# Optimization experiments

Hardware: AMD Instinct MI355X
Metric: run time of the kernel (lower is better)

Reference implementation:

```python
import jax, jax.numpy as jnp
import numpy as np

N, F_IN, HEADS, F_OUT = 4096, 128, 4, 32
DENSITY = 0.05


def setup_inputs() -> dict:
    key = jax.random.key(0)
    k_x, k_adj, k_w, k_as, k_ad, k_b = jax.random.split(key, 6)
    x = jax.random.normal(k_x, (N, F_IN), dtype=jnp.float32)
    # binary adjacency with self-loops so every row of Tau_sum is nonzero
    adj = (jax.random.uniform(k_adj, (N, N)) < DENSITY).astype(jnp.float32)
    adj = jnp.maximum(adj, jnp.eye(N, dtype=jnp.float32))
    weight = jax.random.normal(k_w, (HEADS * F_OUT, F_IN), dtype=jnp.float32) * 0.1
    att_src = jax.random.normal(k_as, (1, HEADS, F_OUT), dtype=jnp.float32) * 0.1
    att_dst = jax.random.normal(k_ad, (1, HEADS, F_OUT), dtype=jnp.float32) * 0.1
    bias = jax.random.normal(k_b, (HEADS * F_OUT,), dtype=jnp.float32) * 0.1
    return {"x": x, "adj_matrix": adj, "weight": weight,
            "att_src": att_src, "att_dst": att_dst, "bias": bias}


def reference(x, adj_matrix, weight, att_src, att_dst, bias):
    n = x.shape[0]
    heads = att_src.shape[1]
    f_out = weight.shape[0] // heads
    # H' = x W^T, reshaped to [N, heads, F_out]
    h_prime = (x @ weight.T).reshape(n, heads, f_out)
    alpha_src = jnp.sum(h_prime * att_src, axis=-1)  # [N, heads]
    alpha_dst = jnp.sum(h_prime * att_dst, axis=-1)  # [N, heads]
    # C[m, n, h] = alpha_src[n, h] + alpha_dst[m, h]
    C = alpha_src[None, :, :] + alpha_dst[:, None, :]
    adj_t = adj_matrix.T[..., None]                  # [N, N, 1]
    # exp(leaky_relu(C, 0.2)) masked by adjacency
    tau = adj_t * jnp.exp(jnp.maximum(0.2 * C, C))   # [N, N, heads]
    tau_sum = jnp.sum(tau, axis=1, keepdims=True)    # [N, 1, heads]
    att_weights = tau / tau_sum
    # Z[m, h, f] = sum_n (adjT * att)[m, n, h] * H'[n, h, f]
    z = jnp.einsum('mnh,nhf->mhf', adj_t * att_weights, h_prime)
    return z.reshape(n, heads * f_out) + bias
```

## Files before the change

kernel.cpp:

```cpp
#include <hip/hip_runtime.h>
#include <hip/hip_bf16.h>

#define N_NODES 4096
#define F_IN    128
#define HEADS   4
#define FTOT    128
#define NSPLIT  16
#define NRANGE  (N_NODES / NSPLIT)
#define NSTEP   (NRANGE / 64)
#define HPB     512
#define BITB    1024
#define L2E     1.4426950408889634f

typedef __attribute__((ext_vector_type(8)))  short  short8v;
typedef __attribute__((ext_vector_type(16))) float  float16v;

static __device__ __forceinline__ unsigned f2bfu(float f) {
    union { __hip_bfloat16 h; unsigned short u; } cv;
    cv.h = __float2bfloat16(f);
    return (unsigned)cv.u;
}
static __device__ __forceinline__ unsigned cvt_pk_bf16(float lo, float hi) {
    unsigned r;
    asm("v_cvt_pk_bf16_f32 %0, %1, %2" : "=v"(r) : "v"(lo), "v"(hi));
    return r;
}

__global__ __launch_bounds__(256)
void k_pre(const float* __restrict__ x, const float* __restrict__ W,
           const float* __restrict__ att_src, const float* __restrict__ att_dst,
           const float* __restrict__ adj,
           unsigned short* __restrict__ hpt, float* __restrict__ ast,
           float* __restrict__ adt, unsigned* __restrict__ abits)
{
    const int t = threadIdx.x;
    if (blockIdx.x < HPB) {
        __shared__ alignas(16) float    xs[8 * F_IN];
        __shared__ alignas(16) unsigned hs[F_IN * 4];
        __shared__ float ssa[4][8], ssd[4][8];
        const int sub = t >> 7;
        const int tt  = t & 127;
        const int i0  = blockIdx.x * 8;
        reinterpret_cast<float4*>(xs)[t] =
            reinterpret_cast<const float4*>(x + (size_t)i0 * F_IN)[t];
        __syncthreads();

        const float4* W4  = reinterpret_cast<const float4*>(W + tt * F_IN);
        const float4* xs4 = reinterpret_cast<const float4*>(xs + sub * 4 * F_IN);
        float a0 = 0.f, a1 = 0.f, a2 = 0.f, a3 = 0.f;
#pragma unroll
        for (int k = 0; k < F_IN / 4; ++k) {
            const float4 w  = W4[k];
            const float4 v0 = xs4[k], v1 = xs4[32 + k], v2 = xs4[64 + k], v3 = xs4[96 + k];
            a0 = fmaf(w.x, v0.x, a0); a0 = fmaf(w.y, v0.y, a0); a0 = fmaf(w.z, v0.z, a0); a0 = fmaf(w.w, v0.w, a0);
            a1 = fmaf(w.x, v1.x, a1); a1 = fmaf(w.y, v1.y, a1); a1 = fmaf(w.z, v1.z, a1); a1 = fmaf(w.w, v1.w, a1);
            a2 = fmaf(w.x, v2.x, a2); a2 = fmaf(w.y, v2.y, a2); a2 = fmaf(w.z, v2.z, a2); a2 = fmaf(w.w, v2.w, a2);
            a3 = fmaf(w.x, v3.x, a3); a3 = fmaf(w.y, v3.y, a3); a3 = fmaf(w.z, v3.z, a3); a3 = fmaf(w.w, v3.w, a3);
        }
        hs[tt * 4 + sub * 2 + 0] = f2bfu(a0) | (f2bfu(a1) << 16);
        hs[tt * 4 + sub * 2 + 1] = f2bfu(a2) | (f2bfu(a3) << 16);

        const float asv = att_src[tt], adv = att_dst[tt];
        float s0 = a0 * asv, s1 = a1 * asv, s2 = a2 * asv, s3 = a3 * asv;
        float d0 = a0 * adv, d1 = a1 * adv, d2 = a2 * adv, d3 = a3 * adv;
#pragma unroll
        for (int s = 16; s; s >>= 1) {
            s0 += __shfl_xor(s0, s); s1 += __shfl_xor(s1, s);
            s2 += __shfl_xor(s2, s); s3 += __shfl_xor(s3, s);
            d0 += __shfl_xor(d0, s); d1 += __shfl_xor(d1, s);
            d2 += __shfl_xor(d2, s); d3 += __shfl_xor(d3, s);
        }
        if ((tt & 31) == 0) {
            const int hh = tt >> 5;
            ssa[hh][sub * 4 + 0] = s0 * L2E; ssa[hh][sub * 4 + 1] = s1 * L2E;
            ssa[hh][sub * 4 + 2] = s2 * L2E; ssa[hh][sub * 4 + 3] = s3 * L2E;
            ssd[hh][sub * 4 + 0] = d0 * L2E; ssd[hh][sub * 4 + 1] = d1 * L2E;
            ssd[hh][sub * 4 + 2] = d2 * L2E; ssd[hh][sub * 4 + 3] = d3 * L2E;
        }
        __syncthreads();
        if (t < 128)
            *reinterpret_cast<uint4*>(hpt + (size_t)t * N_NODES + i0) =
                *reinterpret_cast<const uint4*>(&hs[t * 4]);
        if (t < 64) {
            const int sd = t >> 5, hh = (t >> 3) & 3, nn = t & 7;
            const float v = sd ? ssd[hh][nn] : ssa[hh][nn];
            (sd ? adt : ast)[hh * N_NODES + i0 + nn] = v;
        }
    } else {
        __shared__ alignas(16) unsigned short lb[64 * 16];
        const int sblk  = blockIdx.x - HPB;
        const int strip = sblk & 63;
        const int chunk = sblk >> 6;
        const int c0    = strip * 64;
        const int r0    = chunk * 256;
        const int q     = t & 15;
        const int p     = t >> 4;
        const float4* adj4 = reinterpret_cast<const float4*>(adj);

        float4 v[16];
#pragma unroll
        for (int it = 0; it < 16; ++it)
            v[it] = adj4[(size_t)(r0 + p * 16 + it) * (N_NODES / 4) + (c0 >> 2) + q];
        unsigned mk0 = 0, mk1 = 0, mk2 = 0, mk3 = 0;
#pragma unroll
        for (int it = 0; it < 16; ++it) {
            mk0 |= (v[it].x != 0.f) ? (1u << it) : 0u;
            mk1 |= (v[it].y != 0.f) ? (1u << it) : 0u;
            mk2 |= (v[it].z != 0.f) ? (1u << it) : 0u;
            mk3 |= (v[it].w != 0.f) ? (1u << it) : 0u;
        }
        lb[(4 * q + 0) * 16 + p] = (unsigned short)mk0;
        lb[(4 * q + 1) * 16 + p] = (unsigned short)mk1;
        lb[(4 * q + 2) * 16 + p] = (unsigned short)mk2;
        lb[(4 * q + 3) * 16 + p] = (unsigned short)mk3;
        __syncthreads();
        const unsigned* lb32 = reinterpret_cast<const unsigned*>(lb);
#pragma unroll
        for (int j = 0; j < 2; ++j) {
            const int w = t + j * 256;
            const int m = w >> 3, col = w & 7;
            abits[(size_t)(c0 + m) * (N_NODES / 32) + chunk * 8 + col] = lb32[w];
        }
    }
}

__global__ __launch_bounds__(256, 8)
void k_main(const unsigned short* __restrict__ hpt, const float* __restrict__ ast,
            const float* __restrict__ adt, const unsigned* __restrict__ abits,
            unsigned short* __restrict__ zp16, float* __restrict__ taup)
{
    __shared__ alignas(16) float2 ea_s[HEADS * NRANGE];
    const int t     = threadIdx.x;
    const int wv    = t >> 6;
    const int l     = t & 63;
    const int np    = l >> 5;
    const int lm    = l & 31;
    const int mt    = blockIdx.x >> 4;
    const int split = blockIdx.x & 15;
    const int m0    = mt * 32;
    const int nb0   = split * NRANGE;

#pragma unroll
    for (int j = 0; j < 4; ++j) {
        const int lin = j * 256 + t;
        const int h   = lin >> 8;
        const int n   = lin & 255;
        const float a = ast[h * N_NODES + nb0 + n];
        ea_s[lin] = make_float2(__builtin_amdgcn_exp2f(a),
                                __builtin_amdgcn_exp2f(0.2f * a));
    }
    uint4 brow[2];
    {
        const uint4* bsrc = reinterpret_cast<const uint4*>(
            abits + (size_t)(m0 + lm) * (N_NODES / 32) + split * 8);
        brow[0] = bsrc[0];
        brow[1] = bsrc[1];
    }
    const float adm = adt[wv * N_NODES + m0 + lm];
    const float ed1 = __builtin_amdgcn_exp2f(adm);
    const float ed2 = __builtin_amdgcn_exp2f(0.2f * adm);
    __syncthreads();

    const unsigned short* hrow = hpt + (size_t)(wv * 32 + lm) * N_NODES + nb0 + np * 8;
    const float2* eaw = ea_s + wv * NRANGE;

    float16v acc;
#pragma unroll
    for (int r = 0; r < 16; ++r) acc[r] = 0.f;
    float tau = 0.f;

#pragma unroll
    for (int step = 0; step < NSTEP; ++step) {
#pragma unroll
        for (int q = 0; q < 4; ++q) {
            const short8v bv = *reinterpret_cast<const short8v*>(hrow + step * 64 + q * 16);
            const float2* eap = eaw + step * 64 + q * 16 + np * 8;
            const unsigned w32 = (&brow[0].x)[(step * 2 + (q >> 1)) & 7];
            const unsigned bb  = (w32 >> (((q & 1) << 4) + (np << 3))) & 0xFFu;
            float w[8];
#pragma unroll
            for (int i = 0; i < 8; ++i) {
                const float2 e = eap[i];
                const float sel = fmaxf(e.x * ed1, e.y * ed2);
                w[i] = (bb & (1u << i)) ? sel : 0.f;
            }
            const float t01 = w[0] + w[1], t23 = w[2] + w[3];
            const float t45 = w[4] + w[5], t67 = w[6] + w[7];
            tau += (t01 + t23) + (t45 + t67);
            union { short8v v; unsigned u[4]; } af;
            af.u[0] = cvt_pk_bf16(w[0], w[1]);
            af.u[1] = cvt_pk_bf16(w[2], w[3]);
            af.u[2] = cvt_pk_bf16(w[4], w[5]);
            af.u[3] = cvt_pk_bf16(w[6], w[7]);
            acc = __builtin_amdgcn_mfma_f32_32x32x16_bf16(af.v, bv, acc, 0, 0, 0);
        }
    }

    tau += __shfl_xor(tau, 32);
    if (np == 0)
        taup[((size_t)split * HEADS + wv) * N_NODES + m0 + lm] = tau;
    unsigned short* zp = zp16 + (size_t)split * N_NODES * FTOT;
#pragma unroll
    for (int r = 0; r < 16; ++r) {
        const int row = (r & 3) + 8 * (r >> 2) + 4 * np;
        zp[(size_t)(m0 + row) * FTOT + wv * 32 + lm] = (unsigned short)f2bfu(acc[r]);
    }
}

__global__ __launch_bounds__(256)
void k_fin(const unsigned* __restrict__ zp32, const float* __restrict__ taup,
           const float* __restrict__ bias, float* __restrict__ out)
{
    const int idx = blockIdx.x * 256 + threadIdx.x;
    const int m = idx >> 5, f4 = idx & 31, h = f4 >> 3;
    float4 z = make_float4(0.f, 0.f, 0.f, 0.f);
    float ts = 0.f;
#pragma unroll
    for (int s = 0; s < NSPLIT; ++s) {
        const uint2 u = reinterpret_cast<const uint2*>(zp32)[(size_t)s * (N_NODES * FTOT / 4) + idx];
        z.x += __uint_as_float(u.x << 16);
        z.y += __uint_as_float(u.x & 0xffff0000u);
        z.z += __uint_as_float(u.y << 16);
        z.w += __uint_as_float(u.y & 0xffff0000u);
        ts += taup[((size_t)s * HEADS + h) * N_NODES + m];
    }
    const float inv = 1.f / ts;
    const float4 b = reinterpret_cast<const float4*>(bias)[f4];
    float4 o;
    o.x = z.x * inv + b.x; o.y = z.y * inv + b.y;
    o.z = z.z * inv + b.z; o.w = z.w * inv + b.w;
    reinterpret_cast<float4*>(out)[idx] = o;
}

extern "C" void kernel_launch(void* const* d_in, const int* in_sizes, int n_in,
                              void* d_out, int out_size, void* d_ws, size_t ws_size,
                              hipStream_t stream) {
    const float* x       = (const float*)d_in[0];
    const float* adj     = (const float*)d_in[1];
    const float* weight  = (const float*)d_in[2];
    const float* att_src = (const float*)d_in[3];
    const float* att_dst = (const float*)d_in[4];
    const float* bias    = (const float*)d_in[5];
    float* out = (float*)d_out;

    unsigned short* hpt = (unsigned short*)d_ws;
    float* ast = (float*)(hpt + (size_t)FTOT * N_NODES);
    float* adt = ast + (size_t)HEADS * N_NODES;
    unsigned* abits = (unsigned*)(adt + (size_t)HEADS * N_NODES);
    unsigned short* zp16 = (unsigned short*)(abits + (size_t)N_NODES * (N_NODES / 32));
    float* taup = (float*)(zp16 + (size_t)NSPLIT * N_NODES * FTOT);

    k_pre <<<HPB + BITB, 256, 0, stream>>>(x, weight, att_src, att_dst, adj,
                                           hpt, ast, adt, abits);
    k_main<<<(N_NODES / 32) * NSPLIT, 256, 0, stream>>>(hpt, ast, adt, abits,
                                                        zp16, taup);
    k_fin <<<N_NODES * (FTOT / 4) / 256, 256, 0, stream>>>((const unsigned*)zp16,
                                                           taup, bias, out);
}
```

Baseline: 50.11 us.

## Halve split count and use two independent MFMA accumulator chains per wave

Each block now covers twice the neighbor range (NSPLIT 16→8), cutting the partial-sum traffic written by k_main and reduced by k_fin. The range is split into two halves processed in the same loop with separate accumulators and tau sums, giving two independent MFMA dependency chains to hide MFMA latency. The cost is doubled LDS for the exp table, more registers (launch bounds lowered to 4 blocks), and half as many blocks, which reduces occupancy and parallelism.

```diff
diff --git a/kernel.cpp b/kernel.cpp
--- a/kernel.cpp
+++ b/kernel.cpp
@@ -5,9 +5,10 @@
 #define F_IN    128
 #define HEADS   4
 #define FTOT    128
-#define NSPLIT  16
+#define NSPLIT  8
 #define NRANGE  (N_NODES / NSPLIT)
-#define NSTEP   (NRANGE / 64)
+#define NHALF   (NRANGE / 2)
+#define NSTEP   (NHALF / 64)
 #define HPB     512
 #define BITB    1024
 #define L2E     1.4426950408889634f
@@ -124,7 +125,7 @@
     }
 }
 
-__global__ __launch_bounds__(256, 8)
+__global__ __launch_bounds__(256, 4)
 void k_main(const unsigned short* __restrict__ hpt, const float* __restrict__ ast,
             const float* __restrict__ adt, const unsigned* __restrict__ abits,
             unsigned short* __restrict__ zp16, float* __restrict__ taup)
@@ -135,26 +136,26 @@
     const int l     = t & 63;
     const int np    = l >> 5;
     const int lm    = l & 31;
-    const int mt    = blockIdx.x >> 4;
-    const int split = blockIdx.x & 15;
+    const int mt    = blockIdx.x >> 3;
+    const int split = blockIdx.x & 7;
     const int m0    = mt * 32;
     const int nb0   = split * NRANGE;
 
 #pragma unroll
-    for (int j = 0; j < 4; ++j) {
+    for (int j = 0; j < 8; ++j) {
         const int lin = j * 256 + t;
-        const int h   = lin >> 8;
-        const int n   = lin & 255;
+        const int h   = lin >> 9;
+        const int n   = lin & 511;
         const float a = ast[h * N_NODES + nb0 + n];
         ea_s[lin] = make_float2(__builtin_amdgcn_exp2f(a),
                                 __builtin_amdgcn_exp2f(0.2f * a));
     }
-    uint4 brow[2];
+    uint4 brow[4];
     {
         const uint4* bsrc = reinterpret_cast<const uint4*>(
-            abits + (size_t)(m0 + lm) * (N_NODES / 32) + split * 8);
-        brow[0] = bsrc[0];
-        brow[1] = bsrc[1];
+            abits + (size_t)(m0 + lm) * (N_NODES / 32) + split * 16);
+#pragma unroll
+        for (int j = 0; j < 4; ++j) brow[j] = bsrc[j];
     }
     const float adm = adt[wv * N_NODES + m0 + lm];
     const float ed1 = __builtin_amdgcn_exp2f(adm);
@@ -164,38 +165,47 @@
     const unsigned short* hrow = hpt + (size_t)(wv * 32 + lm) * N_NODES + nb0 + np * 8;
     const float2* eaw = ea_s + wv * NRANGE;
 
-    float16v acc;
-#pragma unroll
-    for (int r = 0; r < 16; ++r) acc[r] = 0.f;
-    float tau = 0.f;
+    float16v acc0, acc1;
+#pragma unroll
+    for (int r = 0; r < 16; ++r) { acc0[r] = 0.f; acc1[r] = 0.f; }
+    float tau0 = 0.f, tau1 = 0.f;
 
 #pragma unroll
     for (int step = 0; step < NSTEP; ++step) {
 #pragma unroll
         for (int q = 0; q < 4; ++q) {
-            const short8v bv = *reinterpret_cast<const short8v*>(hrow + step * 64 + q * 16);
-            const float2* eap = eaw + step * 64 + q * 16 + np * 8;
-            const unsigned w32 = (&brow[0].x)[(step * 2 + (q >> 1)) & 7];
-            const unsigned bb  = (w32 >> (((q & 1) << 4) + (np << 3))) & 0xFFu;
-            float w[8];
+            const int nA = step * 64 + q * 16;
+            const int nB = NHALF + nA;
+            const short8v bvA = *reinterpret_cast<const short8v*>(hrow + nA);
+            const short8v bvB = *reinterpret_cast<const short8v*>(hrow + nB);
+            const float2* eapA = eaw + nA + np * 8;
+            const float2* eapB = eaw + nB + np * 8;
+            const unsigned sh  = ((q & 1) << 4) + (np << 3);
+            const unsigned bbA = ((&brow[0].x)[step * 2 + (q >> 1)]     >> sh) & 0xFFu;
+            const unsigned bbB = ((&brow[0].x)[8 + step * 2 + (q >> 1)] >> sh) & 0xFFu;
+            float wA[8], wB[8];
 #pragma unroll
             for (int i = 0; i < 8; ++i) {
-                const float2 e = eap[i];
-                const float sel = fmaxf(e.x * ed1, e.y * ed2);
-                w[i] = (bb & (1u << i)) ? sel : 0.f;
+                const float2 eA = eapA[i];
+                const float2 eB = eapB[i];
+                const float sA = fmaxf(eA.x * ed1, eA.y * ed2);
+                const float sB = fmaxf(eB.x * ed1, eB.y * ed2);
+                wA[i] = (bbA & (1u << i)) ? sA : 0.f;
+                wB[i] = (bbB & (1u << i)) ? sB : 0.f;
             }
-            const float t01 = w[0] + w[1], t23 = w[2] + w[3];
-            const float t45 = w[4] + w[5], t67 = w[6] + w[7];
-            tau += (t01 + t23) + (t45 + t67);
-            union { short8v v; unsigned u[4]; } af;
-            af.u[0] = cvt_pk_bf16(w[0], w[1]);
-            af.u[1] = cvt_pk_bf16(w[2], w[3]);
-            af.u[2] = cvt_pk_bf16(w[4], w[5]);
-            af.u[3] = cvt_pk_bf16(w[6], w[7]);
-            acc = __builtin_amdgcn_mfma_f32_32x32x16_bf16(af.v, bv, acc, 0, 0, 0);
-        }
-    }
-
+            tau0 += ((wA[0] + wA[1]) + (wA[2] + wA[3])) + ((wA[4] + wA[5]) + (wA[6] + wA[7]));
+            tau1 += ((wB[0] + wB[1]) + (wB[2] + wB[3])) + ((wB[4] + wB[5]) + (wB[6] + wB[7]));
+            union { short8v v; unsigned u[4]; } afA, afB;
+            afA.u[0] = cvt_pk_bf16(wA[0], wA[1]); afA.u[1] = cvt_pk_bf16(wA[2], wA[3]);
+            afA.u[2] = cvt_pk_bf16(wA[4], wA[5]); afA.u[3] = cvt_pk_bf16(wA[6], wA[7]);
+            afB.u[0] = cvt_pk_bf16(wB[0], wB[1]); afB.u[1] = cvt_pk_bf16(wB[2], wB[3]);
+            afB.u[2] = cvt_pk_bf16(wB[4], wB[5]); afB.u[3] = cvt_pk_bf16(wB[6], wB[7]);
+            acc0 = __builtin_amdgcn_mfma_f32_32x32x16_bf16(afA.v, bvA, acc0, 0, 0, 0);
+            acc1 = __builtin_amdgcn_mfma_f32_32x32x16_bf16(afB.v, bvB, acc1, 0, 0, 0);
+        }
+    }
+
+    float tau = tau0 + tau1;
     tau += __shfl_xor(tau, 32);
     if (np == 0)
         taup[((size_t)split * HEADS + wv) * N_NODES + m0 + lm] = tau;
@@ -203,7 +213,8 @@
 #pragma unroll
     for (int r = 0; r < 16; ++r) {
         const int row = (r & 3) + 8 * (r >> 2) + 4 * np;
-        zp[(size_t)(m0 + row) * FTOT + wv * 32 + lm] = (unsigned short)f2bfu(acc[r]);
+        zp[(size_t)(m0 + row) * FTOT + wv * 32 + lm] =
+            (unsigned short)f2bfu(acc0[r] + acc1[r]);
     }
 }
 
```

Result: faster. 46.87 us (-6.5%).

## Fuse adjacency bitmask construction into main kernel using ballots with prefetch

Applied to the files above, without the earlier changes.

Removes the separate adjacency-to-bitmask pass from the preprocessing kernel and instead has the main kernel read fp32 adjacency rows directly, building per-lane masks with wave ballots while prefetching the next step's rows. The split count is halved, so each block covers a larger node range with a larger shared exponent table and lower occupancy bound. This removes the bitmask write/read round trip and one phase of work, at the cost of redundant per-wave adjacency loads, narrower 128-byte row segments, and ballot overhead in the hot loop.

```diff
diff --git a/kernel.cpp b/kernel.cpp
--- a/kernel.cpp
+++ b/kernel.cpp
@@ -5,11 +5,9 @@
 #define F_IN    128
 #define HEADS   4
 #define FTOT    128
-#define NSPLIT  16
+#define NSPLIT  8
 #define NRANGE  (N_NODES / NSPLIT)
 #define NSTEP   (NRANGE / 64)
-#define HPB     512
-#define BITB    1024
 #define L2E     1.4426950408889634f
 
 typedef __attribute__((ext_vector_type(8)))  short  short8v;
@@ -29,104 +27,66 @@
 __global__ __launch_bounds__(256)
 void k_pre(const float* __restrict__ x, const float* __restrict__ W,
            const float* __restrict__ att_src, const float* __restrict__ att_dst,
-           const float* __restrict__ adj,
            unsigned short* __restrict__ hpt, float* __restrict__ ast,
-           float* __restrict__ adt, unsigned* __restrict__ abits)
+           float* __restrict__ adt)
 {
     const int t = threadIdx.x;
-    if (blockIdx.x < HPB) {
-        __shared__ alignas(16) float    xs[8 * F_IN];
-        __shared__ alignas(16) unsigned hs[F_IN * 4];
-        __shared__ float ssa[4][8], ssd[4][8];
-        const int sub = t >> 7;
-        const int tt  = t & 127;
-        const int i0  = blockIdx.x * 8;
-        reinterpret_cast<float4*>(xs)[t] =
-            reinterpret_cast<const float4*>(x + (size_t)i0 * F_IN)[t];
-        __syncthreads();
-
-        const float4* W4  = reinterpret_cast<const float4*>(W + tt * F_IN);
-        const float4* xs4 = reinterpret_cast<const float4*>(xs + sub * 4 * F_IN);
-        float a0 = 0.f, a1 = 0.f, a2 = 0.f, a3 = 0.f;
-#pragma unroll
-        for (int k = 0; k < F_IN / 4; ++k) {
-            const float4 w  = W4[k];
-            const float4 v0 = xs4[k], v1 = xs4[32 + k], v2 = xs4[64 + k], v3 = xs4[96 + k];
-            a0 = fmaf(w.x, v0.x, a0); a0 = fmaf(w.y, v0.y, a0); a0 = fmaf(w.z, v0.z, a0); a0 = fmaf(w.w, v0.w, a0);
-            a1 = fmaf(w.x, v1.x, a1); a1 = fmaf(w.y, v1.y, a1); a1 = fmaf(w.z, v1.z, a1); a1 = fmaf(w.w, v1.w, a1);
-            a2 = fmaf(w.x, v2.x, a2); a2 = fmaf(w.y, v2.y, a2); a2 = fmaf(w.z, v2.z, a2); a2 = fmaf(w.w, v2.w, a2);
-            a3 = fmaf(w.x, v3.x, a3); a3 = fmaf(w.y, v3.y, a3); a3 = fmaf(w.z, v3.z, a3); a3 = fmaf(w.w, v3.w, a3);
-        }
-        hs[tt * 4 + sub * 2 + 0] = f2bfu(a0) | (f2bfu(a1) << 16);
-        hs[tt * 4 + sub * 2 + 1] = f2bfu(a2) | (f2bfu(a3) << 16);
-
-        const float asv = att_src[tt], adv = att_dst[tt];
-        float s0 = a0 * asv, s1 = a1 * asv, s2 = a2 * asv, s3 = a3 * asv;
-        float d0 = a0 * adv, d1 = a1 * adv, d2 = a2 * adv, d3 = a3 * adv;
-#pragma unroll
-        for (int s = 16; s; s >>= 1) {
-            s0 += __shfl_xor(s0, s); s1 += __shfl_xor(s1, s);
-            s2 += __shfl_xor(s2, s); s3 += __shfl_xor(s3, s);
-            d0 += __shfl_xor(d0, s); d1 += __shfl_xor(d1, s);
-            d2 += __shfl_xor(d2, s); d3 += __shfl_xor(d3, s);
-        }
-        if ((tt & 31) == 0) {
-            const int hh = tt >> 5;
-            ssa[hh][sub * 4 + 0] = s0 * L2E; ssa[hh][sub * 4 + 1] = s1 * L2E;
-            ssa[hh][sub * 4 + 2] = s2 * L2E; ssa[hh][sub * 4 + 3] = s3 * L2E;
-            ssd[hh][sub * 4 + 0] = d0 * L2E; ssd[hh][sub * 4 + 1] = d1 * L2E;
-            ssd[hh][sub * 4 + 2] = d2 * L2E; ssd[hh][sub * 4 + 3] = d3 * L2E;
-        }
-        __syncthreads();
-        if (t < 128)
-            *reinterpret_cast<uint4*>(hpt + (size_t)t * N_NODES + i0) =
-                *reinterpret_cast<const uint4*>(&hs[t * 4]);
-        if (t < 64) {
-            const int sd = t >> 5, hh = (t >> 3) & 3, nn = t & 7;
-            const float v = sd ? ssd[hh][nn] : ssa[hh][nn];
-            (sd ? adt : ast)[hh * N_NODES + i0 + nn] = v;
-        }
-    } else {
-        __shared__ alignas(16) unsigned short lb[64 * 16];
-        const int sblk  = blockIdx.x - HPB;
-        const int strip = sblk & 63;
-        const int chunk = sblk >> 6;
-        const int c0    = strip * 64;
-        const int r0    = chunk * 256;
-        const int q     = t & 15;
-        const int p     = t >> 4;
-        const float4* adj4 = reinterpret_cast<const float4*>(adj);
-
-        float4 v[16];
-#pragma unroll
-        for (int it = 0; it < 16; ++it)
-            v[it] = adj4[(size_t)(r0 + p * 16 + it) * (N_NODES / 4) + (c0 >> 2) + q];
-        unsigned mk0 = 0, mk1 = 0, mk2 = 0, mk3 = 0;
-#pragma unroll
-        for (int it = 0; it < 16; ++it) {
-            mk0 |= (v[it].x != 0.f) ? (1u << it) : 0u;
-            mk1 |= (v[it].y != 0.f) ? (1u << it) : 0u;
-            mk2 |= (v[it].z != 0.f) ? (1u << it) : 0u;
-            mk3 |= (v[it].w != 0.f) ? (1u << it) : 0u;
-        }
-        lb[(4 * q + 0) * 16 + p] = (unsigned short)mk0;
-        lb[(4 * q + 1) * 16 + p] = (unsigned short)mk1;
-        lb[(4 * q + 2) * 16 + p] = (unsigned short)mk2;
-        lb[(4 * q + 3) * 16 + p] = (unsigned short)mk3;
-        __syncthreads();
-        const unsigned* lb32 = reinterpret_cast<const unsigned*>(lb);
-#pragma unroll
-        for (int j = 0; j < 2; ++j) {
-            const int w = t + j * 256;
-            const int m = w >> 3, col = w & 7;
-            abits[(size_t)(c0 + m) * (N_NODES / 32) + chunk * 8 + col] = lb32[w];
-        }
-    }
-}
-
-__global__ __launch_bounds__(256, 8)
+    __shared__ alignas(16) float    xs[8 * F_IN];
+    __shared__ alignas(16) unsigned hs[F_IN * 4];
+    __shared__ float ssa[4][8], ssd[4][8];
+    const int sub = t >> 7;
+    const int tt  = t & 127;
+    const int i0  = blockIdx.x * 8;
+    reinterpret_cast<float4*>(xs)[t] =
+        reinterpret_cast<const float4*>(x + (size_t)i0 * F_IN)[t];
+    __syncthreads();
+
+    const float4* W4  = reinterpret_cast<const float4*>(W + tt * F_IN);
+    const float4* xs4 = reinterpret_cast<const float4*>(xs + sub * 4 * F_IN);
+    float a0 = 0.f, a1 = 0.f, a2 = 0.f, a3 = 0.f;
+#pragma unroll
+    for (int k = 0; k < F_IN / 4; ++k) {
+        const float4 w  = W4[k];
+        const float4 v0 = xs4[k], v1 = xs4[32 + k], v2 = xs4[64 + k], v3 = xs4[96 + k];
+        a0 = fmaf(w.x, v0.x, a0); a0 = fmaf(w.y, v0.y, a0); a0 = fmaf(w.z, v0.z, a0); a0 = fmaf(w.w, v0.w, a0);
+        a1 = fmaf(w.x, v1.x, a1); a1 = fmaf(w.y, v1.y, a1); a1 = fmaf(w.z, v1.z, a1); a1 = fmaf(w.w, v1.w, a1);
+        a2 = fmaf(w.x, v2.x, a2); a2 = fmaf(w.y, v2.y, a2); a2 = fmaf(w.z, v2.z, a2); a2 = fmaf(w.w, v2.w, a2);
+        a3 = fmaf(w.x, v3.x, a3); a3 = fmaf(w.y, v3.y, a3); a3 = fmaf(w.z, v3.z, a3); a3 = fmaf(w.w, v3.w, a3);
+    }
+    hs[tt * 4 + sub * 2 + 0] = f2bfu(a0) | (f2bfu(a1) << 16);
+    hs[tt * 4 + sub * 2 + 1] = f2bfu(a2) | (f2bfu(a3) << 16);
+
+    const float asv = att_src[tt], adv = att_dst[tt];
+    float s0 = a0 * asv, s1 = a1 * asv, s2 = a2 * asv, s3 = a3 * asv;
+    float d0 = a0 * adv, d1 = a1 * adv, d2 = a2 * adv, d3 = a3 * adv;
+#pragma unroll
+    for (int s = 16; s; s >>= 1) {
+        s0 += __shfl_xor(s0, s); s1 += __shfl_xor(s1, s);
+        s2 += __shfl_xor(s2, s); s3 += __shfl_xor(s3, s);
+        d0 += __shfl_xor(d0, s); d1 += __shfl_xor(d1, s);
+        d2 += __shfl_xor(d2, s); d3 += __shfl_xor(d3, s);
+    }
+    if ((tt & 31) == 0) {
+        const int hh = tt >> 5;
+        ssa[hh][sub * 4 + 0] = s0 * L2E; ssa[hh][sub * 4 + 1] = s1 * L2E;
+        ssa[hh][sub * 4 + 2] = s2 * L2E; ssa[hh][sub * 4 + 3] = s3 * L2E;
+        ssd[hh][sub * 4 + 0] = d0 * L2E; ssd[hh][sub * 4 + 1] = d1 * L2E;
+        ssd[hh][sub * 4 + 2] = d2 * L2E; ssd[hh][sub * 4 + 3] = d3 * L2E;
+    }
+    __syncthreads();
+    if (t < 128)
+        *reinterpret_cast<uint4*>(hpt + (size_t)t * N_NODES + i0) =
+            *reinterpret_cast<const uint4*>(&hs[t * 4]);
+    if (t < 64) {
+        const int sd = t >> 5, hh = (t >> 3) & 3, nn = t & 7;
+        const float v = sd ? ssd[hh][nn] : ssa[hh][nn];
+        (sd ? adt : ast)[hh * N_NODES + i0 + nn] = v;
+    }
+}
+
+__global__ __launch_bounds__(256, 4)
 void k_main(const unsigned short* __restrict__ hpt, const float* __restrict__ ast,
-            const float* __restrict__ adt, const unsigned* __restrict__ abits,
+            const float* __restrict__ adt, const float* __restrict__ adj,
             unsigned short* __restrict__ zp16, float* __restrict__ taup)
 {
     __shared__ alignas(16) float2 ea_s[HEADS * NRANGE];
@@ -135,32 +95,26 @@
     const int l     = t & 63;
     const int np    = l >> 5;
     const int lm    = l & 31;
-    const int mt    = blockIdx.x >> 4;
-    const int split = blockIdx.x & 15;
+    const int mt    = blockIdx.x >> 3;
+    const int split = blockIdx.x & 7;
     const int m0    = mt * 32;
     const int nb0   = split * NRANGE;
 
 #pragma unroll
-    for (int j = 0; j < 4; ++j) {
+    for (int j = 0; j < 8; ++j) {
         const int lin = j * 256 + t;
-        const int h   = lin >> 8;
-        const int n   = lin & 255;
+        const int h   = lin >> 9;
+        const int n   = lin & 511;
         const float a = ast[h * N_NODES + nb0 + n];
         ea_s[lin] = make_float2(__builtin_amdgcn_exp2f(a),
                                 __builtin_amdgcn_exp2f(0.2f * a));
-    }
-    uint4 brow[2];
-    {
-        const uint4* bsrc = reinterpret_cast<const uint4*>(
-            abits + (size_t)(m0 + lm) * (N_NODES / 32) + split * 8);
-        brow[0] = bsrc[0];
-        brow[1] = bsrc[1];
     }
     const float adm = adt[wv * N_NODES + m0 + lm];
     const float ed1 = __builtin_amdgcn_exp2f(adm);
     const float ed2 = __builtin_amdgcn_exp2f(0.2f * adm);
     __syncthreads();
 
+    const float4* adjr = reinterpret_cast<const float4*>(adj);
     const unsigned short* hrow = hpt + (size_t)(wv * 32 + lm) * N_NODES + nb0 + np * 8;
     const float2* eaw = ea_s + wv * NRANGE;
 
@@ -169,14 +123,38 @@
     for (int r = 0; r < 16; ++r) acc[r] = 0.f;
     float tau = 0.f;
 
-#pragma unroll
+    float4 rv[8];
+#define LOADROWS(step_) do {                                                   \
+        const size_t base_ = (size_t)(nb0 + (step_) * 64 + l) * (N_NODES / 4)  \
+                             + (m0 >> 2);                                      \
+        _Pragma("unroll")                                                      \
+        for (int j_ = 0; j_ < 8; ++j_) rv[j_] = adjr[base_ + j_];              \
+    } while (0)
+
+    auto mkbits = [&]() -> unsigned long long {
+        unsigned long long sel = 0;
+#pragma unroll
+        for (int j = 0; j < 8; ++j) {
+            unsigned long long b;
+            b = __ballot(rv[j].x != 0.f); if (lm == 4 * j + 0) sel = b;
+            b = __ballot(rv[j].y != 0.f); if (lm == 4 * j + 1) sel = b;
+            b = __ballot(rv[j].z != 0.f); if (lm == 4 * j + 2) sel = b;
+            b = __ballot(rv[j].w != 0.f); if (lm == 4 * j + 3) sel = b;
+        }
+        return sel;
+    };
+
+    LOADROWS(0);
+    unsigned long long bits = mkbits();
+
     for (int step = 0; step < NSTEP; ++step) {
+        if (step + 1 < NSTEP) LOADROWS(step + 1);
 #pragma unroll
         for (int q = 0; q < 4; ++q) {
-            const short8v bv = *reinterpret_cast<const short8v*>(hrow + step * 64 + q * 16);
-            const float2* eap = eaw + step * 64 + q * 16 + np * 8;
-            const unsigned w32 = (&brow[0].x)[(step * 2 + (q >> 1)) & 7];
-            const unsigned bb  = (w32 >> (((q & 1) << 4) + (np << 3))) & 0xFFu;
+            const int nq = step * 64 + q * 16;
+            const short8v bv = *reinterpret_cast<const short8v*>(hrow + nq);
+            const float2* eap = eaw + nq + np * 8;
+            const unsigned bb = (unsigned)(bits >> ((2 * q + np) * 8)) & 0xFFu;
             float w[8];
 #pragma unroll
             for (int i = 0; i < 8; ++i) {
@@ -184,9 +162,7 @@
                 const float sel = fmaxf(e.x * ed1, e.y * ed2);
                 w[i] = (bb & (1u << i)) ? sel : 0.f;
             }
-            const float t01 = w[0] + w[1], t23 = w[2] + w[3];
-            const float t45 = w[4] + w[5], t67 = w[6] + w[7];
-            tau += (t01 + t23) + (t45 + t67);
+            tau += ((w[0] + w[1]) + (w[2] + w[3])) + ((w[4] + w[5]) + (w[6] + w[7]));
             union { short8v v; unsigned u[4]; } af;
             af.u[0] = cvt_pk_bf16(w[0], w[1]);
             af.u[1] = cvt_pk_bf16(w[2], w[3]);
@@ -194,7 +170,9 @@
             af.u[3] = cvt_pk_bf16(w[6], w[7]);
             acc = __builtin_amdgcn_mfma_f32_32x32x16_bf16(af.v, bv, acc, 0, 0, 0);
         }
-    }
+        if (step + 1 < NSTEP) bits = mkbits();
+    }
+#undef LOADROWS
 
     tau += __shfl_xor(tau, 32);
     if (np == 0)
@@ -246,13 +224,12 @@
     unsigned short* hpt = (unsigned short*)d_ws;
     float* ast = (float*)(hpt + (size_t)FTOT * N_NODES);
     float* adt = ast + (size_t)HEADS * N_NODES;
-    unsigned* abits = (unsigned*)(adt + (size_t)HEADS * N_NODES);
-    unsigned short* zp16 = (unsigned short*)(abits + (size_t)N_NODES * (N_NODES / 32));
+    unsigned short* zp16 = (unsigned short*)(adt + (size_t)HEADS * N_NODES);
     float* taup = (float*)(zp16 + (size_t)NSPLIT * N_NODES * FTOT);
 
-    k_pre <<<HPB + BITB, 256, 0, stream>>>(x, weight, att_src, att_dst, adj,
-                                           hpt, ast, adt, abits);
-    k_main<<<(N_NODES / 32) * NSPLIT, 256, 0, stream>>>(hpt, ast, adt, abits,
+    k_pre <<<N_NODES / 8, 256, 0, stream>>>(x, weight, att_src, att_dst,
+                                            hpt, ast, adt);
+    k_main<<<(N_NODES / 32) * NSPLIT, 256, 0, stream>>>(hpt, ast, adt, adj,
                                                         zp16, taup);
     k_fin <<<N_NODES * (FTOT / 4) / 256, 256, 0, stream>>>((const unsigned*)zp16,
                                                            taup, bias, out);
```

After: 70.26 us. 40.2% more time.

## Precompute source exponentials in prologue and halve split count in main kernel

Applied to the files above, without the earlier changes.

The per-source exp2 pair (for the leaky-relu branches) is now computed once in k_pre and stored as a float2 table, instead of every k_main block recomputing it into shared memory. k_main reads that table directly from global memory, which removes the LDS staging and the __syncthreads. NSPLIT drops from 16 to 8, so each block covers twice as many source nodes and the partial z/tau buffers and the final reduction shrink. In exchange there are half as many blocks, the occupancy hint falls to 4, and the exp table is read through cache rather than LDS.

```diff
diff --git a/kernel.cpp b/kernel.cpp
--- a/kernel.cpp
+++ b/kernel.cpp
@@ -5,7 +5,7 @@
 #define F_IN    128
 #define HEADS   4
 #define FTOT    128
-#define NSPLIT  16
+#define NSPLIT  8
 #define NRANGE  (N_NODES / NSPLIT)
 #define NSTEP   (NRANGE / 64)
 #define HPB     512
@@ -30,7 +30,7 @@
 void k_pre(const float* __restrict__ x, const float* __restrict__ W,
            const float* __restrict__ att_src, const float* __restrict__ att_dst,
            const float* __restrict__ adj,
-           unsigned short* __restrict__ hpt, float* __restrict__ ast,
+           unsigned short* __restrict__ hpt, float2* __restrict__ eat,
            float* __restrict__ adt, unsigned* __restrict__ abits)
 {
     const int t = threadIdx.x;
@@ -81,10 +81,14 @@
         if (t < 128)
             *reinterpret_cast<uint4*>(hpt + (size_t)t * N_NODES + i0) =
                 *reinterpret_cast<const uint4*>(&hs[t * 4]);
-        if (t < 64) {
-            const int sd = t >> 5, hh = (t >> 3) & 3, nn = t & 7;
-            const float v = sd ? ssd[hh][nn] : ssa[hh][nn];
-            (sd ? adt : ast)[hh * N_NODES + i0 + nn] = v;
+        if (t < 32) {
+            const int hh = (t >> 3) & 3, nn = t & 7;
+            const float a = ssa[hh][nn];
+            eat[(size_t)hh * N_NODES + i0 + nn] =
+                make_float2(__builtin_amdgcn_exp2f(a), __builtin_amdgcn_exp2f(0.2f * a));
+        } else if (t < 64) {
+            const int hh = (t >> 3) & 3, nn = t & 7;
+            adt[hh * N_NODES + i0 + nn] = ssd[hh][nn];
         }
     } else {
         __shared__ alignas(16) unsigned short lb[64 * 16];
@@ -124,45 +128,34 @@
     }
 }
 
-__global__ __launch_bounds__(256, 8)
-void k_main(const unsigned short* __restrict__ hpt, const float* __restrict__ ast,
+__global__ __launch_bounds__(256, 4)
+void k_main(const unsigned short* __restrict__ hpt, const float2* __restrict__ eat,
             const float* __restrict__ adt, const unsigned* __restrict__ abits,
             unsigned short* __restrict__ zp16, float* __restrict__ taup)
 {
-    __shared__ alignas(16) float2 ea_s[HEADS * NRANGE];
     const int t     = threadIdx.x;
     const int wv    = t >> 6;
     const int l     = t & 63;
     const int np    = l >> 5;
     const int lm    = l & 31;
-    const int mt    = blockIdx.x >> 4;
-    const int split = blockIdx.x & 15;
+    const int mt    = blockIdx.x >> 3;
+    const int split = blockIdx.x & 7;
     const int m0    = mt * 32;
     const int nb0   = split * NRANGE;
 
-#pragma unroll
-    for (int j = 0; j < 4; ++j) {
-        const int lin = j * 256 + t;
-        const int h   = lin >> 8;
-        const int n   = lin & 255;
-        const float a = ast[h * N_NODES + nb0 + n];
-        ea_s[lin] = make_float2(__builtin_amdgcn_exp2f(a),
-                                __builtin_amdgcn_exp2f(0.2f * a));
-    }
-    uint4 brow[2];
+    uint4 brow[4];
     {
         const uint4* bsrc = reinterpret_cast<const uint4*>(
-            abits + (size_t)(m0 + lm) * (N_NODES / 32) + split * 8);
-        brow[0] = bsrc[0];
-        brow[1] = bsrc[1];
+            abits + (size_t)(m0 + lm) * (N_NODES / 32) + split * 16);
+#pragma unroll
+        for (int j = 0; j < 4; ++j) brow[j] = bsrc[j];
     }
     const float adm = adt[wv * N_NODES + m0 + lm];
     const float ed1 = __builtin_amdgcn_exp2f(adm);
     const float ed2 = __builtin_amdgcn_exp2f(0.2f * adm);
-    __syncthreads();
 
     const unsigned short* hrow = hpt + (size_t)(wv * 32 + lm) * N_NODES + nb0 + np * 8;
-    const float2* eaw = ea_s + wv * NRANGE;
+    const float2* eaw = eat + (size_t)wv * N_NODES + nb0;
 
     float16v acc;
 #pragma unroll
@@ -173,9 +166,10 @@
     for (int step = 0; step < NSTEP; ++step) {
 #pragma unroll
         for (int q = 0; q < 4; ++q) {
-            const short8v bv = *reinterpret_cast<const short8v*>(hrow + step * 64 + q * 16);
-            const float2* eap = eaw + step * 64 + q * 16 + np * 8;
-            const unsigned w32 = (&brow[0].x)[(step * 2 + (q >> 1)) & 7];
+            const int nq = step * 64 + q * 16;
+            const short8v bv = *reinterpret_cast<const short8v*>(hrow + nq);
+            const float2* eap = eaw + nq + np * 8;
+            const unsigned w32 = (&brow[0].x)[(step * 2 + (q >> 1)) & 15];
             const unsigned bb  = (w32 >> (((q & 1) << 4) + (np << 3))) & 0xFFu;
             float w[8];
 #pragma unroll
@@ -184,9 +178,7 @@
                 const float sel = fmaxf(e.x * ed1, e.y * ed2);
                 w[i] = (bb & (1u << i)) ? sel : 0.f;
             }
-            const float t01 = w[0] + w[1], t23 = w[2] + w[3];
-            const float t45 = w[4] + w[5], t67 = w[6] + w[7];
-            tau += (t01 + t23) + (t45 + t67);
+            tau += ((w[0] + w[1]) + (w[2] + w[3])) + ((w[4] + w[5]) + (w[6] + w[7]));
             union { short8v v; unsigned u[4]; } af;
             af.u[0] = cvt_pk_bf16(w[0], w[1]);
             af.u[1] = cvt_pk_bf16(w[2], w[3]);
@@ -244,15 +236,15 @@
     float* out = (float*)d_out;
 
     unsigned short* hpt = (unsigned short*)d_ws;
-    float* ast = (float*)(hpt + (size_t)FTOT * N_NODES);
-    float* adt = ast + (size_t)HEADS * N_NODES;
+    float2* eat = (float2*)(hpt + (size_t)FTOT * N_NODES);
+    float* adt = (float*)(eat + (size_t)HEADS * N_NODES);
     unsigned* abits = (unsigned*)(adt + (size_t)HEADS * N_NODES);
     unsigned short* zp16 = (unsigned short*)(abits + (size_t)N_NODES * (N_NODES / 32));
     float* taup = (float*)(zp16 + (size_t)NSPLIT * N_NODES * FTOT);
 
     k_pre <<<HPB + BITB, 256, 0, stream>>>(x, weight, att_src, att_dst, adj,
-                                           hpt, ast, adt, abits);
-    k_main<<<(N_NODES / 32) * NSPLIT, 256, 0, stream>>>(hpt, ast, adt, abits,
+                                           hpt, eat, adt, abits);
+    k_main<<<(N_NODES / 32) * NSPLIT, 256, 0, stream>>>(hpt, eat, adt, abits,
                                                         zp16, taup);
     k_fin <<<N_NODES * (FTOT / 4) / 256, 256, 0, stream>>>((const unsigned*)zp16,
                                                            taup, bias, out);
```

Measured after the change: 58.43 us. +16.6%, slower.
